# Performance work log

Measured on AMD Instinct MI355X. Metric: run time of the kernel, lower is better.

Reference implementation:

```python
import jax, jax.numpy as jnp
import numpy as np

B, S, D = 4, 1024, 1024
H, DK, DH = 16, 64, 64  # num_heads, key_size, head_size
NEG = 1e12


def setup_inputs() -> dict:
    key = jax.random.key(0)
    ks = jax.random.split(key, 16)
    scale = 0.02
    inp = {
        'q': jax.random.normal(ks[0], (B, S, D), jnp.float32),
        'k': jax.random.normal(ks[1], (B, S, D), jnp.float32),
        'v': jax.random.normal(ks[2], (B, S, D), jnp.float32),
        'v_mask': jax.random.randint(ks[3], (B, S), 0, 2, jnp.int32),
        'q_mask': jax.random.randint(ks[4], (B, S), 0, 2, jnp.int32),
        # causal attention mask (float, 1 = keep)
        'a_mask': jnp.tril(jnp.ones((S, S), jnp.float32))[None, None, :, :],
        'Wq': jax.random.normal(ks[5], (D, H * DK), jnp.float32) * scale,
        'bq': jnp.zeros((H * DK,), jnp.float32),
        'Wk': jax.random.normal(ks[6], (D, H * DK), jnp.float32) * scale,
        'bk': jnp.zeros((H * DK,), jnp.float32),
        'Wv': jax.random.normal(ks[7], (D, H * DH), jnp.float32) * scale,
        'bv': jnp.zeros((H * DH,), jnp.float32),
        'Wo': jax.random.normal(ks[8], (H * DH, H * DH), jnp.float32) * scale,
        'bo': jnp.zeros((H * DH,), jnp.float32),
    }
    return inp


def reference(q, k, v, v_mask, q_mask, a_mask, Wq, bq, Wk, bk, Wv, bv, Wo, bo):
    b, sq, _ = q.shape
    sk = k.shape[1]
    qw = (jnp.einsum('bsd,de->bse', q, Wq) + bq).reshape(b, sq, H, DK)
    kw = (jnp.einsum('bsd,de->bse', k, Wk) + bk).reshape(b, sk, H, DK)
    vw = (jnp.einsum('bsd,de->bse', v, Wv) + bv).reshape(b, sk, H, DH)
    # scores [b, h, sq, sk]
    a = jnp.einsum('bjhd,bkhd->bhjk', qw, kw) / jnp.sqrt(jnp.float32(DK))
    vm = v_mask.astype(jnp.float32)  # [b, sk]
    a = a - (1.0 - vm)[:, None, None, :] * NEG  # sequence_masking mode='add'
    a = a - (1.0 - a_mask) * NEG                # attention mask
    p = jax.nn.softmax(a, axis=-1)
    o = jnp.einsum('bhjk,bkhd->bjhd', p, vw).reshape(b, sq, H * DH)
    o = jnp.einsum('bse,ef->bsf', o, Wo) + bo
    qm = q_mask.astype(jnp.float32)
    o = o * qm[:, :, None]  # sequence_masking mode='mul'
    return o
```

## Files before the change

kernel.cpp:

```cpp
#include <hip/hip_runtime.h>
#include <cstdint>
#include <cstddef>

typedef unsigned short u16;
using short8 = __attribute__((ext_vector_type(8))) short;
using f32x4  = __attribute__((ext_vector_type(4))) float;

constexpr int Sc = 1024;
constexpr float PEN = 60.0f;

__device__ __forceinline__ u16 f2bf(float f) {
  union { float f; uint32_t u; } v; v.f = f;
  return (u16)((v.u + 0x7fffu + ((v.u >> 16) & 1u)) >> 16);
}

__device__ __forceinline__ void gload_lds16(const u16* g, u16* l) {
  __builtin_amdgcn_global_load_lds(
      (const __attribute__((address_space(1))) uint32_t*)g,
      (__attribute__((address_space(3))) uint32_t*)l, 16, 0, 0);
}

__device__ __forceinline__ f32x4 mfma16(short8 a, short8 b, f32x4 c) {
  return __builtin_amdgcn_mfma_f32_16x16x32_bf16(a, b, c, 0, 0, 0);
}

__global__ __launch_bounds__(256) void prep(
    const float* __restrict__ q, const float* __restrict__ k,
    const float* __restrict__ v, u16* __restrict__ qb, u16* __restrict__ kb,
    u16* __restrict__ vb, const float* __restrict__ W0,
    const float* __restrict__ W1, const float* __restrict__ W2,
    const float* __restrict__ W3, u16* __restrict__ D0, u16* __restrict__ D1,
    u16* __restrict__ D2, u16* __restrict__ D3) {
  const int y = blockIdx.y;
  if (y < 3) {
    const float* src = y == 0 ? q : y == 1 ? k : v;
    u16* dst = y == 0 ? qb : y == 1 ? kb : vb;
    int i = blockIdx.x * 256 + threadIdx.x;
    float4 a = ((const float4*)src)[2 * i];
    float4 b = ((const float4*)src)[2 * i + 1];
    u16 t[8] = {f2bf(a.x), f2bf(a.y), f2bf(a.z), f2bf(a.w),
                f2bf(b.x), f2bf(b.y), f2bf(b.z), f2bf(b.w)};
    ((uint4*)dst)[i] = *(const uint4*)t;
  } else {
    if (blockIdx.x >= 1024) return;
    const int z = y - 3;
    const float* W = z == 0 ? W0 : z == 1 ? W1 : z == 2 ? W2 : W3;
    u16* WT = z == 0 ? D0 : z == 1 ? D1 : z == 2 ? D2 : D3;
    __shared__ float t[32][33];
    int bx = (blockIdx.x & 31) * 32, by = (blockIdx.x >> 5) * 32;
    int tx = threadIdx.x & 31, ty = threadIdx.x >> 5;
    for (int i = 0; i < 32; i += 8)
      t[ty + i][tx] = W[(size_t)(by + ty + i) * 1024 + bx + tx];
    __syncthreads();
    for (int i = 0; i < 32; i += 8)
      WT[(size_t)(bx + ty + i) * 1024 + by + tx] = f2bf(t[tx][ty + i]);
  }
}

__global__ __launch_bounds__(256, 6) void gemm_qkv(
    const u16* __restrict__ qb, const u16* __restrict__ kb,
    const u16* __restrict__ vb, const u16* __restrict__ BT,
    const float* __restrict__ bq, const float* __restrict__ bk,
    const float* __restrict__ bv, u16* __restrict__ QW, u16* __restrict__ KW,
    u16* __restrict__ VTg) {
  const int bid = blockIdx.x;
  const int xcd = bid & 7, local = bid >> 3;
  const int mp = local & 3, nbi = local >> 2;
  const int m0 = (xcd * 4 + mp) * 128, n0 = nbi * 64;
  const int seg = nbi >> 4;
  const u16* A    = seg == 0 ? qb : seg == 1 ? kb : vb;
  const float* bias = seg == 0 ? bq : seg == 1 ? bk : bv;

  __shared__ u16 As0[128 * 32], As1[128 * 32];
  __shared__ u16 Bs0[64 * 32], Bs1[64 * 32];

  const int t = threadIdx.x, w = t >> 6, lane = t & 63;
  const int q4 = lane >> 4, lm = lane & 15;
  const int wm = (w >> 1) * 64, wn = (w & 1) * 32;
  const int srow = lane >> 2, p = lane & 3;
  const int cf = q4 ^ ((lm >> 2) & 3);

  const int rbA0 = (w * 2) * 16, rbA1 = (w * 2 + 1) * 16, rbB = w * 16;
  const int rowA0 = rbA0 + srow, rowA1 = rbA1 + srow, rowB = rbB + srow;
  const int cA0 = p ^ ((rowA0 >> 2) & 3), cA1 = p ^ ((rowA1 >> 2) & 3);
  const int cB = p ^ ((rowB >> 2) & 3);
  const u16* pa0 = &A[(size_t)(m0 + rowA0) * 1024 + cA0 * 8];
  const u16* pa1 = &A[(size_t)(m0 + rowA1) * 1024 + cA1 * 8];
  const u16* pb  = &BT[(size_t)(n0 + rowB) * 1024 + cB * 8];

  f32x4 acc[4][2] = {};

  auto stage = [&](u16* as, u16* bs) {
    gload_lds16(pa0, as + rbA0 * 32);
    gload_lds16(pa1, as + rbA1 * 32);
    gload_lds16(pb, bs + rbB * 32);
    pa0 += 32; pa1 += 32; pb += 32;
  };
  auto compute = [&](const u16* as, const u16* bs) {
    short8 af[4], bf[2];
    for (int mi = 0; mi < 4; ++mi)
      af[mi] = *(const short8*)&as[(wm + mi * 16 + lm) * 32 + cf * 8];
    for (int ni = 0; ni < 2; ++ni)
      bf[ni] = *(const short8*)&bs[(wn + ni * 16 + lm) * 32 + cf * 8];
    for (int mi = 0; mi < 4; ++mi)
      for (int ni = 0; ni < 2; ++ni)
        acc[mi][ni] = mfma16(af[mi], bf[ni], acc[mi][ni]);
  };

  stage(As0, Bs0);
  for (int it = 0; it < 16; ++it) {
    __syncthreads();
    stage(As1, Bs1);
    compute(As0, Bs0);
    __syncthreads();
    if (it < 15) stage(As0, Bs0);
    compute(As1, Bs1);
  }

  if (seg < 2) {
    u16* C = seg == 0 ? QW : KW;
    for (int mi = 0; mi < 4; ++mi)
      for (int ni = 0; ni < 2; ++ni)
        for (int r = 0; r < 4; ++r) {
          int row = m0 + wm + mi * 16 + q4 * 4 + r;
          int col = (n0 + wn + ni * 16 + lm) & 1023;
          C[(size_t)row * 1024 + col] = f2bf(acc[mi][ni][r] + bias[col]);
        }
  } else {
    for (int mi = 0; mi < 4; ++mi)
      for (int ni = 0; ni < 2; ++ni) {
        int row0 = m0 + wm + mi * 16 + q4 * 4;
        int col = (n0 + wn + ni * 16 + lm) & 1023;
        float bv4 = bias[col];
        u16 o4[4];
        for (int r = 0; r < 4; ++r) o4[r] = f2bf(acc[mi][ni][r] + bv4);
        *(uint2*)&VTg[(size_t)col * 4096 + row0] = *(const uint2*)o4;
      }
  }
}

__global__ __launch_bounds__(256, 4) void gemm_out(
    const u16* __restrict__ A, const u16* __restrict__ BT,
    const float* __restrict__ bias, const int* __restrict__ qmask,
    float* __restrict__ Cf) {
  const int bid = blockIdx.x;
  const int xcd = bid & 7, local = bid >> 3;
  const int mp = local & 7, nb = local >> 3;
  const int m0 = (xcd * 8 + mp) * 64, n0 = nb * 64;

  __shared__ u16 As0[64 * 32], As1[64 * 32];
  __shared__ u16 Bs0[64 * 32], Bs1[64 * 32];
  const int t = threadIdx.x, w = t >> 6, lane = t & 63;
  const int q4 = lane >> 4, lm = lane & 15;
  const int wm = (w >> 1) * 32, wn = (w & 1) * 32;
  const int srow = lane >> 2, p = lane & 3;
  const int cf = q4 ^ ((lm >> 2) & 3);

  const int rb = w * 16;
  const int rowS = rb + srow;
  const int cS = p ^ ((rowS >> 2) & 3);
  const u16* pa = &A[(size_t)(m0 + rowS) * 1024 + cS * 8];
  const u16* pb = &BT[(size_t)(n0 + rowS) * 1024 + cS * 8];

  f32x4 acc[2][2] = {};

  auto stage = [&](u16* as, u16* bs) {
    gload_lds16(pa, as + rb * 32);
    gload_lds16(pb, bs + rb * 32);
    pa += 32; pb += 32;
  };
  auto compute = [&](const u16* as, const u16* bs) {
    short8 af[2], bf[2];
    for (int mi = 0; mi < 2; ++mi)
      af[mi] = *(const short8*)&as[(wm + mi * 16 + lm) * 32 + cf * 8];
    for (int ni = 0; ni < 2; ++ni)
      bf[ni] = *(const short8*)&bs[(wn + ni * 16 + lm) * 32 + cf * 8];
    for (int mi = 0; mi < 2; ++mi)
      for (int ni = 0; ni < 2; ++ni)
        acc[mi][ni] = mfma16(af[mi], bf[ni], acc[mi][ni]);
  };

  stage(As0, Bs0);
  for (int it = 0; it < 16; ++it) {
    __syncthreads();
    stage(As1, Bs1);
    compute(As0, Bs0);
    __syncthreads();
    if (it < 15) stage(As0, Bs0);
    compute(As1, Bs1);
  }

  for (int mi = 0; mi < 2; ++mi)
    for (int ni = 0; ni < 2; ++ni)
      for (int r = 0; r < 4; ++r) {
        int row = m0 + wm + mi * 16 + q4 * 4 + r;
        int col = n0 + wn + ni * 16 + lm;
        Cf[(size_t)row * 1024 + col] =
            (acc[mi][ni][r] + bias[col]) * (float)qmask[row];
      }
}

__global__ __launch_bounds__(128, 4) void attn(
    const u16* __restrict__ QW, const u16* __restrict__ KW,
    const u16* __restrict__ VTg, const int* __restrict__ vmask,
    u16* __restrict__ O) {
  const int bid = blockIdx.x;
  const int qtidx = bid >> 7;
  const int qt = qtidx == 0 ? 0 : 16 - qtidx;
  const int rem = bid & 127;
  const int half = rem >> 6, bh = rem & 63;
  const int b = bh >> 4, h = bh & 15;
  const int t = threadIdx.x, w = t >> 6, lane = t & 63;
  const int q4 = lane >> 4, lm = lane & 15;

  __shared__ u16 Ks[2][64 * 64];
  __shared__ u16 P[2][16 * 72];
  __shared__ unsigned char penb[1024];
  __shared__ int anyf;

  if (t == 0) anyf = 0;
  {
    int4 vm0 = ((const int4*)(vmask + b * 1024))[2 * t];
    int4 vm1 = ((const int4*)(vmask + b * 1024))[2 * t + 1];
    unsigned char m8[8] = {
        (unsigned char)(vm0.x == 0), (unsigned char)(vm0.y == 0),
        (unsigned char)(vm0.z == 0), (unsigned char)(vm0.w == 0),
        (unsigned char)(vm1.x == 0), (unsigned char)(vm1.y == 0),
        (unsigned char)(vm1.z == 0), (unsigned char)(vm1.w == 0)};
    *(uint2*)&penb[8 * t] = *(const uint2*)m8;
  }
  __syncthreads();
  {
    int any = 0;
    for (int i = t; i <= qt * 64; i += 128) any |= (penb[i] == 0);
    if (any) atomicOr(&anyf, 1);
  }
  __syncthreads();
  const int ext = !anyf;
  const int kend = ext ? 15 : qt;

  const int qrow0 = qt * 64 + half * 32 + w * 16;
  short8 qf[2];
  {
    const u16* qp = &QW[(size_t)(b * Sc + qrow0 + lm) * 1024 + h * 64];
    qf[0] = *(const short8*)&qp[q4 * 8];
    qf[1] = *(const short8*)&qp[32 + q4 * 8];
    for (int fi = 0; fi < 2; ++fi)
      for (int i = 0; i < 8; ++i) {
        u16 x = (u16)qf[fi][i];
        int e = (x >> 7) & 0xff;
        qf[fi][i] = (short)(e > 3 ? (u16)(x - 0x180) : (u16)(x & 0x8000));
      }
  }

  float l_run[4] = {};
  f32x4 oacc[4] = {};
  const int qrow00 = qrow0 + q4 * 4;

  const u16* Vbase = &VTg[(size_t)(h * 64) * 4096 + b * Sc];
  u16* Pw = &P[w][0];

  const int r0 = lane >> 3, pos = lane & 7, ch = pos ^ r0;
  auto stageK = [&](int kt, int buf) {
    for (int j = 0; j < 4; ++j) {
      int issue = w * 4 + j;
      int row = issue * 8 + r0;
      gload_lds16(&KW[(size_t)(b * Sc + kt * 64 + row) * 1024 + h * 64 + ch * 8],
                  &Ks[buf][issue * 512]);
    }
  };

  stageK(0, 0);
  int cur = 0;
  for (int kt = 0; kt <= kend; ++kt) {
    __syncthreads();
    if (kt < kend) stageK(kt + 1, cur ^ 1);

    short8 vf0[4], vf1[4];
    for (int ni = 0; ni < 4; ++ni) {
      const u16* vp = Vbase + (size_t)(ni * 16 + lm) * 4096 + kt * 64;
      vf0[ni] = *(const short8*)&vp[q4 * 8];
      vf1[ni] = *(const short8*)&vp[32 + q4 * 8];
    }

    const int mode = kt > qt ? 2 : (kt == qt ? 1 : 0);
    f32x4 sacc[4] = {};
    __builtin_amdgcn_s_setprio(1);
    for (int ni = 0; ni < 4; ++ni) {
      int row = ni * 16 + lm;
      short8 kf0 = *(const short8*)&Ks[cur][row * 64 + ((q4 ^ (lm & 7)) * 8)];
      short8 kf1 = *(const short8*)&Ks[cur][row * 64 + (((4 + q4) ^ (lm & 7)) * 8)];
      sacc[ni] = mfma16(qf[0], kf0, sacc[ni]);
      sacc[ni] = mfma16(qf[1], kf1, sacc[ni]);
    }
    __builtin_amdgcn_s_setprio(0);

    for (int ni = 0; ni < 4; ++ni) {
      int key = kt * 64 + ni * 16 + lm;
      float pen = penb[key] ? PEN : 0.0f;
      if (mode == 2) pen += PEN;
      for (int r = 0; r < 4; ++r) {
        float x = sacc[ni][r] - pen;
        if (mode == 1 && key > qrow00 + r) x -= PEN;
        float pv = __expf(x);
        l_run[r] += pv;
        Pw[(q4 * 4 + r) * 72 + ni * 16 + lm] = f2bf(pv);
      }
    }
    short8 pf0 = *(const short8*)&Pw[lm * 72 + q4 * 8];
    short8 pf1 = *(const short8*)&Pw[lm * 72 + 32 + q4 * 8];
    __builtin_amdgcn_s_setprio(1);
    for (int ni = 0; ni < 4; ++ni) {
      oacc[ni] = mfma16(pf0, vf0[ni], oacc[ni]);
      oacc[ni] = mfma16(pf1, vf1[ni], oacc[ni]);
    }
    __builtin_amdgcn_s_setprio(0);
    cur ^= 1;
  }

  for (int r = 0; r < 4; ++r) {
    float l = l_run[r];
    for (int off = 1; off < 16; off <<= 1) l += __shfl_xor(l, off, 64);
    l_run[r] = 1.0f / l;
  }
  for (int ni = 0; ni < 4; ++ni)
    for (int r = 0; r < 4; ++r) {
      int row = b * Sc + qrow00 + r;
      O[(size_t)row * 1024 + h * 64 + ni * 16 + lm] =
          f2bf(oacc[ni][r] * l_run[r]);
    }
}

extern "C" void kernel_launch(void* const* d_in, const int* in_sizes, int n_in,
                              void* d_out, int out_size, void* d_ws, size_t ws_size,
                              hipStream_t stream) {
  (void)in_sizes; (void)n_in; (void)out_size; (void)ws_size;
  const float* q  = (const float*)d_in[0];
  const float* k  = (const float*)d_in[1];
  const float* v  = (const float*)d_in[2];
  const int* vmask = (const int*)d_in[3];
  const int* qmask = (const int*)d_in[4];
  const float* Wq = (const float*)d_in[6];
  const float* bq = (const float*)d_in[7];
  const float* Wk = (const float*)d_in[8];
  const float* bk = (const float*)d_in[9];
  const float* Wv = (const float*)d_in[10];
  const float* bv = (const float*)d_in[11];
  const float* Wo = (const float*)d_in[12];
  const float* bo = (const float*)d_in[13];

  char* ws = (char*)d_ws;
  u16* WT3 = (u16*)ws;
  u16* WoT = (u16*)(ws + 6291456);
  u16* QW  = (u16*)(ws + 8388608);
  u16* KW  = (u16*)(ws + 16777216);
  u16* VTg = (u16*)(ws + 25165824);
  u16* Oat = (u16*)(ws + 33554432);
  u16* qb = (u16*)d_out;
  u16* kb = (u16*)d_out + 4194304;
  u16* vb = Oat;

  dim3 tb(256);
  prep<<<dim3(2048, 7), tb, 0, stream>>>(q, k, v, qb, kb, vb, Wq, Wk, Wv, Wo,
                                         WT3, WT3 + 1048576, WT3 + 2097152,
                                         WoT);
  gemm_qkv<<<dim3(1536), tb, 0, stream>>>(qb, kb, vb, WT3, bq, bk, bv, QW, KW,
                                          VTg);
  attn<<<dim3(2048), dim3(128), 0, stream>>>(QW, KW, VTg, vmask, Oat);
  gemm_out<<<dim3(1024), tb, 0, stream>>>(Oat, WoT, bo, qmask, (float*)d_out);
}
```

Before: 229.2 us.

## Load K fragments directly into registers with double-buffering, dropping LDS staging

Replaces the LDS-staged, double-buffered K tile (global_load_lds plus a per-tile __syncthreads) with direct global loads of K fragments into two register buffers, prefetching the next tile while the current one is processed. The aim is to remove the block barrier and LDS traffic from the inner loop. The cost is 16 extra short8 registers per thread, so launch bounds drop from 4 to 3 blocks per CU. Each wave now loads K separately instead of sharing one staged tile, which doubles K global/L2 traffic.

```diff
diff --git a/kernel.cpp b/kernel.cpp
--- a/kernel.cpp
+++ b/kernel.cpp
@@ -200,7 +200,7 @@
       }
 }
 
-__global__ __launch_bounds__(128, 4) void attn(
+__global__ __launch_bounds__(128, 3) void attn(
     const u16* __restrict__ QW, const u16* __restrict__ KW,
     const u16* __restrict__ VTg, const int* __restrict__ vmask,
     u16* __restrict__ O) {
@@ -213,7 +213,6 @@
   const int t = threadIdx.x, w = t >> 6, lane = t & 63;
   const int q4 = lane >> 4, lm = lane & 15;
 
-  __shared__ u16 Ks[2][64 * 64];
   __shared__ u16 P[2][16 * 72];
   __shared__ unsigned char penb[1024];
   __shared__ int anyf;
@@ -257,26 +256,23 @@
   f32x4 oacc[4] = {};
   const int qrow00 = qrow0 + q4 * 4;
 
+  const u16* Kbase = &KW[(size_t)(b * Sc) * 1024 + h * 64];
   const u16* Vbase = &VTg[(size_t)(h * 64) * 4096 + b * Sc];
   u16* Pw = &P[w][0];
 
-  const int r0 = lane >> 3, pos = lane & 7, ch = pos ^ r0;
-  auto stageK = [&](int kt, int buf) {
-    for (int j = 0; j < 4; ++j) {
-      int issue = w * 4 + j;
-      int row = issue * 8 + r0;
-      gload_lds16(&KW[(size_t)(b * Sc + kt * 64 + row) * 1024 + h * 64 + ch * 8],
-                  &Ks[buf][issue * 512]);
-    }
-  };
-
-  stageK(0, 0);
-  int cur = 0;
-  for (int kt = 0; kt <= kend; ++kt) {
-    __syncthreads();
-    if (kt < kend) stageK(kt + 1, cur ^ 1);
-
+  short8 kA[8], kB[8];
+  auto loadK = [&](int kt, short8 (&kf)[8]) {
+#pragma unroll
+    for (int ni = 0; ni < 4; ++ni) {
+      const u16* kp = Kbase + (size_t)(kt * 64 + ni * 16 + lm) * 1024;
+      kf[2 * ni] = *(const short8*)&kp[q4 * 8];
+      kf[2 * ni + 1] = *(const short8*)&kp[32 + q4 * 8];
+    }
+  };
+
+  auto tile = [&](int kt, const short8 (&kf)[8]) {
     short8 vf0[4], vf1[4];
+#pragma unroll
     for (int ni = 0; ni < 4; ++ni) {
       const u16* vp = Vbase + (size_t)(ni * 16 + lm) * 4096 + kt * 64;
       vf0[ni] = *(const short8*)&vp[q4 * 8];
@@ -286,19 +282,19 @@
     const int mode = kt > qt ? 2 : (kt == qt ? 1 : 0);
     f32x4 sacc[4] = {};
     __builtin_amdgcn_s_setprio(1);
-    for (int ni = 0; ni < 4; ++ni) {
-      int row = ni * 16 + lm;
-      short8 kf0 = *(const short8*)&Ks[cur][row * 64 + ((q4 ^ (lm & 7)) * 8)];
-      short8 kf1 = *(const short8*)&Ks[cur][row * 64 + (((4 + q4) ^ (lm & 7)) * 8)];
-      sacc[ni] = mfma16(qf[0], kf0, sacc[ni]);
-      sacc[ni] = mfma16(qf[1], kf1, sacc[ni]);
+#pragma unroll
+    for (int ni = 0; ni < 4; ++ni) {
+      sacc[ni] = mfma16(qf[0], kf[2 * ni], sacc[ni]);
+      sacc[ni] = mfma16(qf[1], kf[2 * ni + 1], sacc[ni]);
     }
     __builtin_amdgcn_s_setprio(0);
 
+#pragma unroll
     for (int ni = 0; ni < 4; ++ni) {
       int key = kt * 64 + ni * 16 + lm;
       float pen = penb[key] ? PEN : 0.0f;
       if (mode == 2) pen += PEN;
+#pragma unroll
       for (int r = 0; r < 4; ++r) {
         float x = sacc[ni][r] - pen;
         if (mode == 1 && key > qrow00 + r) x -= PEN;
@@ -310,12 +306,23 @@
     short8 pf0 = *(const short8*)&Pw[lm * 72 + q4 * 8];
     short8 pf1 = *(const short8*)&Pw[lm * 72 + 32 + q4 * 8];
     __builtin_amdgcn_s_setprio(1);
+#pragma unroll
     for (int ni = 0; ni < 4; ++ni) {
       oacc[ni] = mfma16(pf0, vf0[ni], oacc[ni]);
       oacc[ni] = mfma16(pf1, vf1[ni], oacc[ni]);
     }
     __builtin_amdgcn_s_setprio(0);
-    cur ^= 1;
+  };
+
+  loadK(0, kA);
+  int kt = 0;
+  while (true) {
+    if (kt < kend) loadK(kt + 1, kB);
+    tile(kt, kA);
+    if (++kt > kend) break;
+    if (kt < kend) loadK(kt + 1, kA);
+    tile(kt, kB);
+    if (++kt > kend) break;
   }
 
   for (int r = 0; r < 4; ++r) {
```

Result: slower. 259.4 us (+13.2%).

## Split attention into single-wave blocks with 32-key tiles and causal-tight bounds

Applied to the files above, without the earlier changes.

The attention kernel now runs one 64-thread wave per block over a 16-row query strip, with 4096 blocks instead of 2048 two-wave blocks. Keys are processed in 32-key tiles, so the causal diagonal is handled at finer granularity and fewer fully masked tiles are computed. Barriers are replaced by explicit vmcnt waits plus a ballot for the any-valid check. The cost is more blocks, more redundant per-block mask staging, and reliance on hand-counted waitcnt values for correctness of the K double buffer.

```diff
diff --git a/kernel.cpp b/kernel.cpp
--- a/kernel.cpp
+++ b/kernel.cpp
@@ -200,49 +200,44 @@
       }
 }
 
-__global__ __launch_bounds__(128, 4) void attn(
+__global__ __launch_bounds__(64, 4) void attn(
     const u16* __restrict__ QW, const u16* __restrict__ KW,
     const u16* __restrict__ VTg, const int* __restrict__ vmask,
     u16* __restrict__ O) {
   const int bid = blockIdx.x;
-  const int qtidx = bid >> 7;
+  const int qtidx = bid >> 8;
   const int qt = qtidx == 0 ? 0 : 16 - qtidx;
-  const int rem = bid & 127;
-  const int half = rem >> 6, bh = rem & 63;
+  const int rem = bid & 255;
+  const int quarter = 3 - (rem >> 6);
+  const int bh = rem & 63;
   const int b = bh >> 4, h = bh & 15;
-  const int t = threadIdx.x, w = t >> 6, lane = t & 63;
+  const int lane = threadIdx.x;
   const int q4 = lane >> 4, lm = lane & 15;
 
-  __shared__ u16 Ks[2][64 * 64];
-  __shared__ u16 P[2][16 * 72];
+  __shared__ u16 Ks[2][32 * 64];
+  __shared__ u16 P[16 * 40];
   __shared__ unsigned char penb[1024];
-  __shared__ int anyf;
-
-  if (t == 0) anyf = 0;
+
   {
-    int4 vm0 = ((const int4*)(vmask + b * 1024))[2 * t];
-    int4 vm1 = ((const int4*)(vmask + b * 1024))[2 * t + 1];
-    unsigned char m8[8] = {
-        (unsigned char)(vm0.x == 0), (unsigned char)(vm0.y == 0),
-        (unsigned char)(vm0.z == 0), (unsigned char)(vm0.w == 0),
-        (unsigned char)(vm1.x == 0), (unsigned char)(vm1.y == 0),
-        (unsigned char)(vm1.z == 0), (unsigned char)(vm1.w == 0)};
-    *(uint2*)&penb[8 * t] = *(const uint2*)m8;
-  }
-  __syncthreads();
-  {
-    int any = 0;
-    for (int i = t; i <= qt * 64; i += 128) any |= (penb[i] == 0);
-    if (any) atomicOr(&anyf, 1);
-  }
-  __syncthreads();
-  const int ext = !anyf;
-  const int kend = ext ? 15 : qt;
-
-  const int qrow0 = qt * 64 + half * 32 + w * 16;
+    const int4* vmp = (const int4*)(vmask + b * 1024);
+    for (int j = 0; j < 4; ++j) {
+      int4 vm = vmp[4 * lane + j];
+      unsigned char m4[4] = {
+          (unsigned char)(vm.x == 0), (unsigned char)(vm.y == 0),
+          (unsigned char)(vm.z == 0), (unsigned char)(vm.w == 0)};
+      *(unsigned int*)&penb[16 * lane + 4 * j] = *(const unsigned int*)m4;
+    }
+  }
+  int any = 0;
+  for (int i = lane; i <= qt * 64; i += 64) any |= (penb[i] == 0);
+  const int ext = (__ballot(any) == 0);
+  const int T = 2 * qt + (quarter >> 1);
+  const int kend = ext ? 31 : T;
+
+  const int R = qt * 64 + quarter * 16;
   short8 qf[2];
   {
-    const u16* qp = &QW[(size_t)(b * Sc + qrow0 + lm) * 1024 + h * 64];
+    const u16* qp = &QW[(size_t)(b * Sc + R + lm) * 1024 + h * 64];
     qf[0] = *(const short8*)&qp[q4 * 8];
     qf[1] = *(const short8*)&qp[32 + q4 * 8];
     for (int fi = 0; fi < 2; ++fi)
@@ -255,67 +250,69 @@
 
   float l_run[4] = {};
   f32x4 oacc[4] = {};
-  const int qrow00 = qrow0 + q4 * 4;
-
+  const int qrow00 = R + q4 * 4;
+
+  const u16* Kbase = &KW[(size_t)(b * Sc) * 1024 + h * 64];
   const u16* Vbase = &VTg[(size_t)(h * 64) * 4096 + b * Sc];
-  u16* Pw = &P[w][0];
 
   const int r0 = lane >> 3, pos = lane & 7, ch = pos ^ r0;
   auto stageK = [&](int kt, int buf) {
     for (int j = 0; j < 4; ++j) {
-      int issue = w * 4 + j;
-      int row = issue * 8 + r0;
-      gload_lds16(&KW[(size_t)(b * Sc + kt * 64 + row) * 1024 + h * 64 + ch * 8],
-                  &Ks[buf][issue * 512]);
+      int row = j * 8 + r0;
+      gload_lds16(Kbase + (size_t)(kt * 32 + row) * 1024 + ch * 8,
+                  &Ks[buf][j * 512]);
     }
   };
 
   stageK(0, 0);
-  int cur = 0;
   for (int kt = 0; kt <= kend; ++kt) {
-    __syncthreads();
-    if (kt < kend) stageK(kt + 1, cur ^ 1);
-
-    short8 vf0[4], vf1[4];
-    for (int ni = 0; ni < 4; ++ni) {
-      const u16* vp = Vbase + (size_t)(ni * 16 + lm) * 4096 + kt * 64;
-      vf0[ni] = *(const short8*)&vp[q4 * 8];
-      vf1[ni] = *(const short8*)&vp[32 + q4 * 8];
-    }
-
-    const int mode = kt > qt ? 2 : (kt == qt ? 1 : 0);
-    f32x4 sacc[4] = {};
+    const int buf = kt & 1;
+    short8 vf[4];
+#pragma unroll
+    for (int ni = 0; ni < 4; ++ni)
+      vf[ni] = *(const short8*)(Vbase + (size_t)(ni * 16 + lm) * 4096 +
+                                kt * 32 + q4 * 8);
+    if (kt < kend) {
+      stageK(kt + 1, buf ^ 1);
+      asm volatile("s_waitcnt vmcnt(8)" ::: "memory");
+    } else {
+      asm volatile("s_waitcnt vmcnt(4)" ::: "memory");
+    }
+    __builtin_amdgcn_sched_barrier(0);
+
+    const int mode = kt > T ? 2 : (kt == T ? 1 : 0);
+    f32x4 sacc[2] = {};
     __builtin_amdgcn_s_setprio(1);
-    for (int ni = 0; ni < 4; ++ni) {
+#pragma unroll
+    for (int ni = 0; ni < 2; ++ni) {
       int row = ni * 16 + lm;
-      short8 kf0 = *(const short8*)&Ks[cur][row * 64 + ((q4 ^ (lm & 7)) * 8)];
-      short8 kf1 = *(const short8*)&Ks[cur][row * 64 + (((4 + q4) ^ (lm & 7)) * 8)];
+      short8 kf0 = *(const short8*)&Ks[buf][row * 64 + ((q4 ^ (lm & 7)) * 8)];
+      short8 kf1 = *(const short8*)&Ks[buf][row * 64 + (((4 + q4) ^ (lm & 7)) * 8)];
       sacc[ni] = mfma16(qf[0], kf0, sacc[ni]);
       sacc[ni] = mfma16(qf[1], kf1, sacc[ni]);
     }
     __builtin_amdgcn_s_setprio(0);
 
-    for (int ni = 0; ni < 4; ++ni) {
-      int key = kt * 64 + ni * 16 + lm;
+#pragma unroll
+    for (int ni = 0; ni < 2; ++ni) {
+      int key = kt * 32 + ni * 16 + lm;
       float pen = penb[key] ? PEN : 0.0f;
       if (mode == 2) pen += PEN;
+#pragma unroll
       for (int r = 0; r < 4; ++r) {
         float x = sacc[ni][r] - pen;
         if (mode == 1 && key > qrow00 + r) x -= PEN;
         float pv = __expf(x);
         l_run[r] += pv;
-        Pw[(q4 * 4 + r) * 72 + ni * 16 + lm] = f2bf(pv);
+        P[(q4 * 4 + r) * 40 + ni * 16 + lm] = f2bf(pv);
       }
     }
-    short8 pf0 = *(const short8*)&Pw[lm * 72 + q4 * 8];
-    short8 pf1 = *(const short8*)&Pw[lm * 72 + 32 + q4 * 8];
+    short8 pf = *(const short8*)&P[lm * 40 + q4 * 8];
     __builtin_amdgcn_s_setprio(1);
-    for (int ni = 0; ni < 4; ++ni) {
-      oacc[ni] = mfma16(pf0, vf0[ni], oacc[ni]);
-      oacc[ni] = mfma16(pf1, vf1[ni], oacc[ni]);
-    }
+#pragma unroll
+    for (int ni = 0; ni < 4; ++ni)
+      oacc[ni] = mfma16(pf, vf[ni], oacc[ni]);
     __builtin_amdgcn_s_setprio(0);
-    cur ^= 1;
   }
 
   for (int r = 0; r < 4; ++r) {
@@ -366,6 +363,6 @@
                                          WoT);
   gemm_qkv<<<dim3(1536), tb, 0, stream>>>(qb, kb, vb, WT3, bq, bk, bv, QW, KW,
                                           VTg);
-  attn<<<dim3(2048), dim3(128), 0, stream>>>(QW, KW, VTg, vmask, Oat);
+  attn<<<dim3(4096), dim3(64), 0, stream>>>(QW, KW, VTg, vmask, Oat);
   gemm_out<<<dim3(1024), tb, 0, stream>>>(Oat, WoT, bo, qmask, (float*)d_out);
 }
```

Result: no change. 232.5 us (+1.4%).
